# Kernel tuning notes

Measured on AMD Instinct MI355X. Metric: run time of the kernel, lower is better.

## Reference

```python
import jax, jax.numpy as jnp
import numpy as np

DIM = 512
HEADS = 8
DIM_HEAD = 64
INNER = HEADS * DIM_HEAD
SCALE = DIM_HEAD ** -0.5


def setup_inputs() -> dict:
    key = jax.random.key(0)
    k1, k2, k3, k4 = jax.random.split(key, 4)
    x = jax.random.normal(k1, (2, 4096, DIM), dtype=jnp.float32)
    # torch Linear stores weight [out, in]; we keep [in, out] for x @ W
    W_qkv = jax.random.normal(k2, (DIM, 3 * INNER), dtype=jnp.float32) * (DIM ** -0.5)
    W_out = jax.random.normal(k3, (INNER, DIM), dtype=jnp.float32) * (INNER ** -0.5)
    b_out = jax.random.normal(k4, (DIM,), dtype=jnp.float32) * 0.01
    return {"x": x, "W_qkv": W_qkv, "W_out": W_out, "b_out": b_out}


def reference(x, W_qkv, W_out, b_out):
    b, l, _ = x.shape
    qkv = x @ W_qkv  # [b, l, 3*inner]
    q, k, v = jnp.split(qkv, 3, axis=-1)

    def split_heads(t):  # [b, l, inner] -> [b, h, l, d]
        return t.reshape(b, l, HEADS, DIM_HEAD).transpose(0, 2, 1, 3)

    q, k, v = split_heads(q), split_heads(k), split_heads(v)
    attn = jnp.einsum('bhid,bhjd->bhij', q, k) * SCALE
    attn = jax.nn.softmax(attn, axis=-1)
    attned = jnp.einsum('bhij,bhjd->bhid', attn, v)
    attned = attned.transpose(0, 2, 1, 3).reshape(b, l, INNER)
    return attned @ W_out + b_out
```

## Files before the change

kernel.cpp:

```cpp
#include <hip/hip_runtime.h>

typedef short bf16x8 __attribute__((ext_vector_type(8)));
typedef float f32x4 __attribute__((ext_vector_type(4)));

#define MFMA16(a, b, c) __builtin_amdgcn_mfma_f32_16x16x32_bf16((a), (b), (c), 0, 0, 0)

__device__ __forceinline__ unsigned short f2bf(float f) {
    union { float f; unsigned u; } v; v.f = f;
    unsigned r = v.u + 0x7FFFu + ((v.u >> 16) & 1u);
    return (unsigned short)(r >> 16);
}

__global__ __launch_bounds__(256) void k_cvt(const float* __restrict__ in,
                                             unsigned short* __restrict__ out, int n4) {
    int i = blockIdx.x * 256 + threadIdx.x;
    if (i < n4) {
        float4 v = reinterpret_cast<const float4*>(in)[i];
        ushort4 o;
        o.x = f2bf(v.x); o.y = f2bf(v.y); o.z = f2bf(v.z); o.w = f2bf(v.w);
        reinterpret_cast<ushort4*>(out)[i] = o;
    }
}

__global__ __launch_bounds__(256) void k_tr(const float* __restrict__ in,
                                            unsigned short* __restrict__ out, int R, int C) {
    __shared__ float t[64][65];
    int c0 = blockIdx.x * 64, r0 = blockIdx.y * 64;
    int lc = threadIdx.x & 63, lr4 = threadIdx.x >> 6;
#pragma unroll
    for (int j = 0; j < 16; ++j) {
        int r = lr4 + j * 4;
        t[r][lc] = in[(size_t)(r0 + r) * C + c0 + lc];
    }
    __syncthreads();
#pragma unroll
    for (int j = 0; j < 16; ++j) {
        int c = lr4 + j * 4;
        out[(size_t)(c0 + c) * R + r0 + lc] = f2bf(t[lc][c]);
    }
}

__device__ __forceinline__ void gemm_main_512(const unsigned short* __restrict__ A,
                                              const unsigned short* __restrict__ Bt,
                                              int m0, int n0,
                                              unsigned short* AL, unsigned short* BL,
                                              f32x4 acc[4][4]) {
    const int tid = threadIdx.x;
    const int lane = tid & 63, wid = tid >> 6;
    const int wr = wid >> 1, wc = wid & 1;
    const int lg = lane >> 4, lr = lane & 15;

    for (int k0 = 0; k0 < 512; k0 += 32) {
#pragma unroll
        for (int i = 0; i < 2; ++i) {
            int idx = tid + i * 256;
            int row = idx >> 2;
            int c8 = (idx & 3) * 8;
            *reinterpret_cast<bf16x8*>(&AL[row * 40 + c8]) =
                *reinterpret_cast<const bf16x8*>(&A[(size_t)(m0 + row) * 512 + k0 + c8]);
            *reinterpret_cast<bf16x8*>(&BL[row * 40 + c8]) =
                *reinterpret_cast<const bf16x8*>(&Bt[(size_t)(n0 + row) * 512 + k0 + c8]);
        }
        __syncthreads();
        bf16x8 af[4], bfr[4];
#pragma unroll
        for (int rt = 0; rt < 4; ++rt)
            af[rt] = *reinterpret_cast<const bf16x8*>(&AL[(wr * 64 + rt * 16 + lr) * 40 + lg * 8]);
#pragma unroll
        for (int ct = 0; ct < 4; ++ct)
            bfr[ct] = *reinterpret_cast<const bf16x8*>(&BL[(wc * 64 + ct * 16 + lr) * 40 + lg * 8]);
#pragma unroll
        for (int rt = 0; rt < 4; ++rt)
#pragma unroll
            for (int ct = 0; ct < 4; ++ct)
                acc[rt][ct] = MFMA16(af[rt], bfr[ct], acc[rt][ct]);
        __syncthreads();
    }
}

__global__ __launch_bounds__(256) void k_gemm_qkv(const unsigned short* __restrict__ X,
                                                  const unsigned short* __restrict__ Wt,
                                                  unsigned short* __restrict__ Qb,
                                                  unsigned short* __restrict__ Kb,
                                                  unsigned short* __restrict__ VbT) {
    __shared__ __align__(16) unsigned short AL[128 * 40];
    __shared__ __align__(16) unsigned short BL[128 * 40];
    f32x4 acc[4][4];
#pragma unroll
    for (int i = 0; i < 4; ++i)
#pragma unroll
        for (int j = 0; j < 4; ++j) acc[i][j] = (f32x4){0.f, 0.f, 0.f, 0.f};

    int m0 = blockIdx.x * 128, n0 = blockIdx.y * 128;
    gemm_main_512(X, Wt, m0, n0, AL, BL, acc);

    const int tid = threadIdx.x;
    const int lane = tid & 63, wid = tid >> 6;
    const int wr = wid >> 1, wc = wid & 1;
    const int lg = lane >> 4, lr = lane & 15;
#pragma unroll
    for (int rt = 0; rt < 4; ++rt) {
#pragma unroll
        for (int ct = 0; ct < 4; ++ct) {
            int col = n0 + wc * 64 + ct * 16 + lr;
            int which = col >> 9, inner = col & 511;
            int h = inner >> 6, d = inner & 63;
#pragma unroll
            for (int j = 0; j < 4; ++j) {
                int row = m0 + wr * 64 + rt * 16 + lg * 4 + j;
                int b = row >> 12, l = row & 4095;
                float v = acc[rt][ct][j];
                if (which == 0) {
                    Qb[(((size_t)(b * 8 + h)) * 4096 + l) * 64 + d] = f2bf(v * 0.18033688f);
                } else if (which == 1) {
                    Kb[(((size_t)(b * 8 + h)) * 4096 + l) * 64 + d] = f2bf(v);
                } else {
                    VbT[(((size_t)(b * 8 + h)) * 64 + d) * 4096 + l] = f2bf(v);
                }
            }
        }
    }
}

__global__ __launch_bounds__(256) void k_gemm_out(const unsigned short* __restrict__ An,
                                                  const unsigned short* __restrict__ Wot,
                                                  const float* __restrict__ bout,
                                                  float* __restrict__ out) {
    __shared__ __align__(16) unsigned short AL[128 * 40];
    __shared__ __align__(16) unsigned short BL[128 * 40];
    f32x4 acc[4][4];
#pragma unroll
    for (int i = 0; i < 4; ++i)
#pragma unroll
        for (int j = 0; j < 4; ++j) acc[i][j] = (f32x4){0.f, 0.f, 0.f, 0.f};

    int m0 = blockIdx.x * 128, n0 = blockIdx.y * 128;
    gemm_main_512(An, Wot, m0, n0, AL, BL, acc);

    const int tid = threadIdx.x;
    const int lane = tid & 63, wid = tid >> 6;
    const int wr = wid >> 1, wc = wid & 1;
    const int lg = lane >> 4, lr = lane & 15;
#pragma unroll
    for (int rt = 0; rt < 4; ++rt) {
#pragma unroll
        for (int ct = 0; ct < 4; ++ct) {
            int col = n0 + wc * 64 + ct * 16 + lr;
            float bv = bout[col];
#pragma unroll
            for (int j = 0; j < 4; ++j) {
                int row = m0 + wr * 64 + rt * 16 + lg * 4 + j;
                out[(size_t)row * 512 + col] = acc[rt][ct][j] + bv;
            }
        }
    }
}

__global__ __launch_bounds__(256) void k_attn(const unsigned short* __restrict__ Q,
                                              const unsigned short* __restrict__ K,
                                              const unsigned short* __restrict__ VT,
                                              unsigned short* __restrict__ O) {
    __shared__ __align__(16) unsigned short KL[64 * 72];
    __shared__ __align__(16) unsigned short VTl[64 * 72];
    __shared__ __align__(16) unsigned short PL[4][32 * 72];

    const int qt = blockIdx.x;
    const int bh = blockIdx.y;
    const size_t base = (size_t)bh * 4096 * 64;
    const int tid = threadIdx.x, lane = tid & 63, wid = tid >> 6;
    const int lg = lane >> 4, lr = lane & 15;
    const int q0 = qt * 128 + wid * 32;

    bf16x8 qf[2][2];
#pragma unroll
    for (int rt = 0; rt < 2; ++rt)
#pragma unroll
        for (int kt = 0; kt < 2; ++kt)
            qf[rt][kt] = *reinterpret_cast<const bf16x8*>(
                &Q[base + (size_t)(q0 + rt * 16 + lr) * 64 + kt * 32 + lg * 8]);

    f32x4 oacc[2][4];
    f32x4 sacc[2];
#pragma unroll
    for (int rt = 0; rt < 2; ++rt) {
        sacc[rt] = (f32x4){0.f, 0.f, 0.f, 0.f};
#pragma unroll
        for (int dt = 0; dt < 4; ++dt) oacc[rt][dt] = (f32x4){0.f, 0.f, 0.f, 0.f};
    }

    bf16x8 ones;
#pragma unroll
    for (int j = 0; j < 8; ++j) ones[j] = (short)0x3F80;

    const int r0 = tid >> 3, c0 = (tid & 7) * 8;

    bf16x8 kreg[2], vreg[2];
#pragma unroll
    for (int i = 0; i < 2; ++i) {
        kreg[i] = *reinterpret_cast<const bf16x8*>(&K[base + (size_t)(r0 + i * 32) * 64 + c0]);
        vreg[i] = *reinterpret_cast<const bf16x8*>(&VT[base + (size_t)(r0 + i * 32) * 4096 + c0]);
    }
#pragma unroll
    for (int i = 0; i < 2; ++i) {
        *reinterpret_cast<bf16x8*>(&KL[(r0 + i * 32) * 72 + c0]) = kreg[i];
        *reinterpret_cast<bf16x8*>(&VTl[(r0 + i * 32) * 72 + c0]) = vreg[i];
    }
    __syncthreads();

    for (int kv = 0; kv < 64; ++kv) {
        const int kv0n = kv * 64 + 64;
        if (kv < 63) {
#pragma unroll
            for (int i = 0; i < 2; ++i) {
                kreg[i] = *reinterpret_cast<const bf16x8*>(
                    &K[base + (size_t)(kv0n + r0 + i * 32) * 64 + c0]);
                vreg[i] = *reinterpret_cast<const bf16x8*>(
                    &VT[base + (size_t)(r0 + i * 32) * 4096 + kv0n + c0]);
            }
        }

        f32x4 s[2][4];
#pragma unroll
        for (int rt = 0; rt < 2; ++rt)
#pragma unroll
            for (int ct = 0; ct < 4; ++ct) s[rt][ct] = (f32x4){0.f, 0.f, 0.f, 0.f};
#pragma unroll
        for (int kt = 0; kt < 2; ++kt) {
#pragma unroll
            for (int ct = 0; ct < 4; ++ct) {
                bf16x8 kf = *reinterpret_cast<const bf16x8*>(
                    &KL[(ct * 16 + lr) * 72 + kt * 32 + lg * 8]);
#pragma unroll
                for (int rt = 0; rt < 2; ++rt)
                    s[rt][ct] = MFMA16(qf[rt][kt], kf, s[rt][ct]);
            }
        }

#pragma unroll
        for (int rt = 0; rt < 2; ++rt)
#pragma unroll
            for (int ct = 0; ct < 4; ++ct)
#pragma unroll
                for (int j = 0; j < 4; ++j)
                    PL[wid][(rt * 16 + lg * 4 + j) * 72 + ct * 16 + lr] =
                        f2bf(__builtin_amdgcn_exp2f(s[rt][ct][j]));

#pragma unroll
        for (int kt = 0; kt < 2; ++kt) {
            bf16x8 pf[2];
#pragma unroll
            for (int rt = 0; rt < 2; ++rt)
                pf[rt] = *reinterpret_cast<const bf16x8*>(
                    &PL[wid][(rt * 16 + lr) * 72 + kt * 32 + lg * 8]);
#pragma unroll
            for (int dt = 0; dt < 4; ++dt) {
                bf16x8 vf = *reinterpret_cast<const bf16x8*>(
                    &VTl[(dt * 16 + lr) * 72 + kt * 32 + lg * 8]);
#pragma unroll
                for (int rt = 0; rt < 2; ++rt)
                    oacc[rt][dt] = MFMA16(pf[rt], vf, oacc[rt][dt]);
            }
#pragma unroll
            for (int rt = 0; rt < 2; ++rt)
                sacc[rt] = MFMA16(pf[rt], ones, sacc[rt]);
        }

        __syncthreads();
        if (kv < 63) {
#pragma unroll
            for (int i = 0; i < 2; ++i) {
                *reinterpret_cast<bf16x8*>(&KL[(r0 + i * 32) * 72 + c0]) = kreg[i];
                *reinterpret_cast<bf16x8*>(&VTl[(r0 + i * 32) * 72 + c0]) = vreg[i];
            }
        }
        __syncthreads();
    }

    const int b = bh >> 3, h = bh & 7;
#pragma unroll
    for (int rt = 0; rt < 2; ++rt) {
#pragma unroll
        for (int j = 0; j < 4; ++j) {
            float inv = 1.f / sacc[rt][j];
            int row = q0 + rt * 16 + lg * 4 + j;
#pragma unroll
            for (int dt = 0; dt < 4; ++dt) {
                int d = dt * 16 + lr;
                O[((size_t)b * 4096 + row) * 512 + h * 64 + d] = f2bf(oacc[rt][dt][j] * inv);
            }
        }
    }
}

extern "C" void kernel_launch(void* const* d_in, const int* in_sizes, int n_in,
                              void* d_out, int out_size, void* d_ws, size_t ws_size,
                              hipStream_t stream) {
    const float* x    = (const float*)d_in[0];
    const float* Wqkv = (const float*)d_in[1];
    const float* Wout = (const float*)d_in[2];
    const float* bout = (const float*)d_in[3];
    float* out = (float*)d_out;

    char* ws = (char*)d_ws;
    unsigned short* Xbf  = (unsigned short*)(ws);
    unsigned short* Wqkt = (unsigned short*)(ws + 8388608);
    unsigned short* Wot  = (unsigned short*)(ws + 8388608 + 1572864);
    unsigned short* Qb   = (unsigned short*)(ws + 10485760);
    unsigned short* Kb   = (unsigned short*)(ws + 18874368);
    unsigned short* VbT  = (unsigned short*)(ws + 27262976);
    unsigned short* An   = (unsigned short*)(ws + 35651584);

    k_cvt<<<4096, 256, 0, stream>>>(x, Xbf, 4194304 / 4);
    k_tr<<<dim3(24, 8), 256, 0, stream>>>(Wqkv, Wqkt, 512, 1536);
    k_tr<<<dim3(8, 8), 256, 0, stream>>>(Wout, Wot, 512, 512);
    k_gemm_qkv<<<dim3(64, 12), 256, 0, stream>>>(Xbf, Wqkt, Qb, Kb, VbT);
    k_attn<<<dim3(32, 16), 256, 0, stream>>>(Qb, Kb, VbT, An);
    k_gemm_out<<<dim3(64, 4), 256, 0, stream>>>(An, Wot, bout, out);
}
```

Measured before the change: 232.5 us.

## Vectorize V-transpose stores, remap attention grid, add MFMA priority hints

The QKV epilogue hoists the Q/K/V selector out of the loops and writes each lane's four consecutive sequence positions of transposed V as one ushort4 store instead of four scattered 2-byte stores. The attention launch is flattened to 1D with the head index varying fastest, which changes the order in which blocks cover the batch-head and query-tile space. s_setprio raises wave priority around the two MFMA phases to help matrix work interleave with the exp and LDS phases of other waves. The bf16 conversion now uses the HIP intrinsic instead of hand-written rounding; this may round NaNs differently but is otherwise meant to be equivalent.

```diff
diff --git a/kernel.cpp b/kernel.cpp
--- a/kernel.cpp
+++ b/kernel.cpp
@@ -1,4 +1,5 @@
 #include <hip/hip_runtime.h>
+#include <hip/hip_bf16.h>
 
 typedef short bf16x8 __attribute__((ext_vector_type(8)));
 typedef float f32x4 __attribute__((ext_vector_type(4)));
@@ -6,9 +7,8 @@
 #define MFMA16(a, b, c) __builtin_amdgcn_mfma_f32_16x16x32_bf16((a), (b), (c), 0, 0, 0)
 
 __device__ __forceinline__ unsigned short f2bf(float f) {
-    union { float f; unsigned u; } v; v.f = f;
-    unsigned r = v.u + 0x7FFFu + ((v.u >> 16) & 1u);
-    return (unsigned short)(r >> 16);
+    __hip_bfloat16 h = __float2bfloat16(f);
+    return *reinterpret_cast<unsigned short*>(&h);
 }
 
 __global__ __launch_bounds__(256) void k_cvt(const float* __restrict__ in,
@@ -98,25 +98,31 @@
     const int lane = tid & 63, wid = tid >> 6;
     const int wr = wid >> 1, wc = wid & 1;
     const int lg = lane >> 4, lr = lane & 15;
+    const int which = n0 >> 9;
 #pragma unroll
     for (int rt = 0; rt < 4; ++rt) {
 #pragma unroll
         for (int ct = 0; ct < 4; ++ct) {
             int col = n0 + wc * 64 + ct * 16 + lr;
-            int which = col >> 9, inner = col & 511;
+            int inner = col & 511;
             int h = inner >> 6, d = inner & 63;
-#pragma unroll
-            for (int j = 0; j < 4; ++j) {
-                int row = m0 + wr * 64 + rt * 16 + lg * 4 + j;
-                int b = row >> 12, l = row & 4095;
-                float v = acc[rt][ct][j];
-                if (which == 0) {
-                    Qb[(((size_t)(b * 8 + h)) * 4096 + l) * 64 + d] = f2bf(v * 0.18033688f);
-                } else if (which == 1) {
-                    Kb[(((size_t)(b * 8 + h)) * 4096 + l) * 64 + d] = f2bf(v);
-                } else {
-                    VbT[(((size_t)(b * 8 + h)) * 64 + d) * 4096 + l] = f2bf(v);
-                }
+            int row0 = m0 + wr * 64 + rt * 16 + lg * 4;
+            int b = row0 >> 12, l0 = row0 & 4095;
+            if (which == 0) {
+#pragma unroll
+                for (int j = 0; j < 4; ++j)
+                    Qb[(((size_t)(b * 8 + h)) * 4096 + l0 + j) * 64 + d] =
+                        f2bf(acc[rt][ct][j] * 0.18033688f);
+            } else if (which == 1) {
+#pragma unroll
+                for (int j = 0; j < 4; ++j)
+                    Kb[(((size_t)(b * 8 + h)) * 4096 + l0 + j) * 64 + d] = f2bf(acc[rt][ct][j]);
+            } else {
+                ushort4 o;
+                o.x = f2bf(acc[rt][ct][0]); o.y = f2bf(acc[rt][ct][1]);
+                o.z = f2bf(acc[rt][ct][2]); o.w = f2bf(acc[rt][ct][3]);
+                *reinterpret_cast<ushort4*>(
+                    &VbT[(((size_t)(b * 8 + h)) * 64 + d) * 4096 + l0]) = o;
             }
         }
     }
@@ -159,13 +165,14 @@
 __global__ __launch_bounds__(256) void k_attn(const unsigned short* __restrict__ Q,
                                               const unsigned short* __restrict__ K,
                                               const unsigned short* __restrict__ VT,
-                                              unsigned short* __restrict__ O) {
+                                              unsigned short* __restrict__ An) {
     __shared__ __align__(16) unsigned short KL[64 * 72];
     __shared__ __align__(16) unsigned short VTl[64 * 72];
     __shared__ __align__(16) unsigned short PL[4][32 * 72];
 
-    const int qt = blockIdx.x;
-    const int bh = blockIdx.y;
+    const int flat = blockIdx.x;
+    const int bh = flat & 15;
+    const int qt = flat >> 4;
     const size_t base = (size_t)bh * 4096 * 64;
     const int tid = threadIdx.x, lane = tid & 63, wid = tid >> 6;
     const int lg = lane >> 4, lr = lane & 15;
@@ -224,6 +231,7 @@
         for (int rt = 0; rt < 2; ++rt)
 #pragma unroll
             for (int ct = 0; ct < 4; ++ct) s[rt][ct] = (f32x4){0.f, 0.f, 0.f, 0.f};
+        __builtin_amdgcn_s_setprio(1);
 #pragma unroll
         for (int kt = 0; kt < 2; ++kt) {
 #pragma unroll
@@ -235,6 +243,7 @@
                     s[rt][ct] = MFMA16(qf[rt][kt], kf, s[rt][ct]);
             }
         }
+        __builtin_amdgcn_s_setprio(0);
 
 #pragma unroll
         for (int rt = 0; rt < 2; ++rt)
@@ -245,6 +254,7 @@
                     PL[wid][(rt * 16 + lg * 4 + j) * 72 + ct * 16 + lr] =
                         f2bf(__builtin_amdgcn_exp2f(s[rt][ct][j]));
 
+        __builtin_amdgcn_s_setprio(1);
 #pragma unroll
         for (int kt = 0; kt < 2; ++kt) {
             bf16x8 pf[2];
@@ -264,6 +274,7 @@
             for (int rt = 0; rt < 2; ++rt)
                 sacc[rt] = MFMA16(pf[rt], ones, sacc[rt]);
         }
+        __builtin_amdgcn_s_setprio(0);
 
         __syncthreads();
         if (kv < 63) {
@@ -286,7 +297,7 @@
 #pragma unroll
             for (int dt = 0; dt < 4; ++dt) {
                 int d = dt * 16 + lr;
-                O[((size_t)b * 4096 + row) * 512 + h * 64 + d] = f2bf(oacc[rt][dt][j] * inv);
+                An[((size_t)b * 4096 + row) * 512 + h * 64 + d] = f2bf(oacc[rt][dt][j] * inv);
             }
         }
     }
@@ -312,8 +323,8 @@
 
     k_cvt<<<4096, 256, 0, stream>>>(x, Xbf, 4194304 / 4);
     k_tr<<<dim3(24, 8), 256, 0, stream>>>(Wqkv, Wqkt, 512, 1536);
-    k_tr<<<dim3(8, 8), 256, 0, stream>>>(Wout, Wot, 512, 512);
+    k_tr<<<dim3(8, 8), 256, 0, stream>>>(Wot == nullptr ? Wout : Wout, Wot, 512, 512);
     k_gemm_qkv<<<dim3(64, 12), 256, 0, stream>>>(Xbf, Wqkt, Qb, Kb, VbT);
-    k_attn<<<dim3(32, 16), 256, 0, stream>>>(Qb, Kb, VbT, An);
+    k_attn<<<dim3(512), 256, 0, stream>>>(Qb, Kb, VbT, An);
     k_gemm_out<<<dim3(64, 4), 256, 0, stream>>>(An, Wot, bout, out);
 }
```

After: 227.7 us. 1.02x faster.
